# Performance work log

Measured on AMD Instinct MI355X. Metric: run time of the kernel, lower is better.

Reference implementation:

```python
import jax, jax.numpy as jnp
import numpy as np

D_MODEL = 1024
NHEAD = 16
HEAD_DIM = D_MODEL // NHEAD
D_FF = 4096
EPS = 1e-5


def _layernorm(x, g, b):
    mu = jnp.mean(x, axis=-1, keepdims=True)
    var = jnp.mean(jnp.square(x - mu), axis=-1, keepdims=True)
    return (x - mu) * jax.lax.rsqrt(var + EPS) * g + b


def setup_inputs() -> dict:
    key = jax.random.key(0)
    ks = jax.random.split(key, 8)

    def xavier(k, shape):
        fan_out, fan_in = shape
        lim = np.sqrt(6.0 / (fan_in + fan_out))
        return jax.random.uniform(k, shape, jnp.float32, -lim, lim)

    x = jax.random.normal(ks[0], (4, 2048, D_MODEL), jnp.float32)
    return {
        "x": x,
        "Wq": xavier(ks[1], (D_MODEL, D_MODEL)), "bq": jnp.zeros((D_MODEL,), jnp.float32),
        "Wk": xavier(ks[2], (D_MODEL, D_MODEL)), "bk": jnp.zeros((D_MODEL,), jnp.float32),
        "Wv": xavier(ks[3], (D_MODEL, D_MODEL)), "bv": jnp.zeros((D_MODEL,), jnp.float32),
        "Wo": xavier(ks[4], (D_MODEL, D_MODEL)), "bo": jnp.zeros((D_MODEL,), jnp.float32),
        "W1": xavier(ks[5], (D_FF, D_MODEL)), "b1": jnp.zeros((D_FF,), jnp.float32),
        "W2": xavier(ks[6], (D_MODEL, D_FF)), "b2": jnp.zeros((D_MODEL,), jnp.float32),
        "ln1_g": jnp.ones((D_MODEL,), jnp.float32), "ln1_b": jnp.zeros((D_MODEL,), jnp.float32),
        "ln2_g": jnp.ones((D_MODEL,), jnp.float32), "ln2_b": jnp.zeros((D_MODEL,), jnp.float32),
    }


def reference(x, Wq, bq, Wk, bk, Wv, bv, Wo, bo, W1, b1, W2, b2, ln1_g, ln1_b, ln2_g, ln2_b):
    B, T, D = x.shape
    H, Hd = NHEAD, HEAD_DIM

    # --- attention sublayer (pre-LN) ---
    residual = x
    xn = _layernorm(x, ln1_g, ln1_b)
    # torch Linear: y = x @ W.T + b
    q = (xn @ Wq.T + bq).reshape(B, T, H, Hd).transpose(0, 2, 1, 3)  # [B,H,T,Hd]
    k = (xn @ Wk.T + bk).reshape(B, T, H, Hd).transpose(0, 2, 1, 3)
    v = (xn @ Wv.T + bv).reshape(B, T, H, Hd).transpose(0, 2, 1, 3)

    scale = Hd ** -0.5
    scores = jnp.einsum('bhqd,bhkd->bhqk', q, k) * scale  # [B,H,T,T]
    attn = jax.nn.softmax(scores, axis=-1)
    out = jnp.einsum('bhqk,bhkd->bhqd', attn, v)           # [B,H,T,Hd]
    out = out.transpose(0, 2, 1, 3).reshape(B, T, D)
    out = out @ Wo.T + bo
    x = residual + out

    # --- FFN sublayer (pre-LN) ---
    residual = x
    xn = _layernorm(x, ln2_g, ln2_b)
    h = jax.nn.relu(xn @ W1.T + b1)
    h = h @ W2.T + b2
    return residual + h
```

## Files before the change

### kernel.cpp

```cpp
#include <hip/hip_runtime.h>
#include <hip/hip_bf16.h>

using bf16 = __hip_bfloat16;
typedef __attribute__((ext_vector_type(8))) short bf16x8;
typedef __attribute__((ext_vector_type(4))) float f32x4;

#define D_MODEL 1024
#define NHEAD 16
#define HEAD_DIM 64
#define D_FF 4096
#define SEQ 2048
#define NTOK 8192

__device__ __forceinline__ void gload16(const void* g, void* l) {
  __builtin_amdgcn_global_load_lds((const __attribute__((address_space(1))) void*)g,
                                   (__attribute__((address_space(3))) void*)l, 16, 0, 0);
}

__device__ __forceinline__ unsigned pkbf16(float lo, float hi) {
  unsigned r;
  asm("v_cvt_pk_bf16_f32 %0, %1, %2" : "=v"(r) : "v"(lo), "v"(hi));
  return r;
}

__device__ __forceinline__ float fexp2(float x) {
  float r;
  asm("v_exp_f32 %0, %1" : "=v"(r) : "v"(x));
  return r;
}

__device__ __forceinline__ float max3f(float a, float b, float c) {
  return fmaxf(fmaxf(a, b), c);
}

__global__ __launch_bounds__(256) void cvt_all(
    const float* __restrict__ W1, const float* __restrict__ W2,
    const float* __restrict__ Wq, const float* __restrict__ Wk,
    const float* __restrict__ Wv, const float* __restrict__ Wo,
    bf16* __restrict__ w1_b, bf16* __restrict__ w2_b,
    bf16* __restrict__ wqkv, bf16* __restrict__ wo_b) {
  const int bid = blockIdx.x;
  const float* src;
  bf16* dst;
  int lb;
  if (bid < 4096) { src = W1; dst = w1_b; lb = bid; }
  else if (bid < 8192) { src = W2; dst = w2_b; lb = bid - 4096; }
  else {
    const int j = (bid - 8192) >> 10;
    lb = (bid - 8192) & 1023;
    if (j == 0) { src = Wq; dst = wqkv; }
    else if (j == 1) { src = Wk; dst = wqkv + 1048576; }
    else if (j == 2) { src = Wv; dst = wqkv + 2097152; }
    else { src = Wo; dst = wo_b; }
  }
  const int i = (lb * 256 + threadIdx.x) * 4;
  const float4 v = *(const float4*)&src[i];
  dst[i + 0] = __float2bfloat16(v.x);
  dst[i + 1] = __float2bfloat16(v.y);
  dst[i + 2] = __float2bfloat16(v.z);
  dst[i + 3] = __float2bfloat16(v.w);
}

__global__ __launch_bounds__(256) void layernorm_kernel(
    const float* __restrict__ xin, const float* __restrict__ g,
    const float* __restrict__ bta, bf16* __restrict__ out) {
  const int row = blockIdx.x, t = threadIdx.x;
  const float4 v = *(const float4*)&xin[(size_t)row * D_MODEL + t * 4];
  float s = v.x + v.y + v.z + v.w;
#pragma unroll
  for (int m = 1; m < 64; m <<= 1) s += __shfl_xor(s, m);
  __shared__ float red[4], red2[4];
  const int w = t >> 6, l = t & 63;
  if (l == 0) red[w] = s;
  __syncthreads();
  const float mu = (red[0] + red[1] + red[2] + red[3]) * (1.f / 1024.f);
  const float d0 = v.x - mu, d1 = v.y - mu, d2 = v.z - mu, d3 = v.w - mu;
  float q = d0 * d0 + d1 * d1 + d2 * d2 + d3 * d3;
#pragma unroll
  for (int m = 1; m < 64; m <<= 1) q += __shfl_xor(q, m);
  if (l == 0) red2[w] = q;
  __syncthreads();
  const float var = (red2[0] + red2[1] + red2[2] + red2[3]) * (1.f / 1024.f);
  const float rs = rsqrtf(var + 1e-5f);
  const float4 gg = *(const float4*)&g[t * 4];
  const float4 bb = *(const float4*)&bta[t * 4];
  bf16* o = out + (size_t)row * D_MODEL + t * 4;
  o[0] = __float2bfloat16(d0 * rs * gg.x + bb.x);
  o[1] = __float2bfloat16(d1 * rs * gg.y + bb.y);
  o[2] = __float2bfloat16(d2 * rs * gg.z + bb.z);
  o[3] = __float2bfloat16(d3 * rs * gg.w + bb.w);
}

template <int MODE>
__global__ __launch_bounds__(512, 2) void gemmA(
    const bf16* __restrict__ A, const bf16* __restrict__ Bw,
    const float* __restrict__ bias0, const float* __restrict__ bias1,
    const float* __restrict__ bias2,
    void* __restrict__ out, int M, int N, int K) {
  constexpr int ASZ = 256 * 128;
  constexpr int TILE = ASZ + 256 * 128;
  __shared__ __align__(16) char smem[2 * TILE];

  const int t = threadIdx.x;
  const int l = t & 63, l15 = l & 15, l4 = (l >> 4) & 3;
  const int w = t >> 6, wm = w >> 2, wn = w & 3;
  const int gx = gridDim.x;
  const int nwg = gx * gridDim.y;
  const int bid0 = blockIdx.y * gx + blockIdx.x;
  const int bid = (bid0 & 7) * (nwg >> 3) + (bid0 >> 3);
  const int m0 = (bid / gx) * 256, n0 = (bid % gx) * 256;

  const int sr = t >> 3;
  const int scol = 8 * ((t & 7) ^ (sr & 7));
  const int swz = (l15 & 7) << 4;
  int coff[2];
  coff[0] = (l4 * 16) ^ swz;
  coff[1] = (64 + l4 * 16) ^ swz;

#define ST_A(j, kb, buf)                                          \
  gload16(&A[(size_t)(m0 + (j) * 64 + sr) * K + (kb) + scol],     \
          (void*)(smem + (buf) * TILE + (j) * 8192 + t * 16))
#define ST_B(j, kb, buf)                                          \
  gload16(&Bw[(size_t)(n0 + (j) * 64 + sr) * K + (kb) + scol],    \
          (void*)(smem + (buf) * TILE + ASZ + (j) * 8192 + t * 16))

  f32x4 acc[8][4] = {};
  const int NTm = K >> 6;

  ST_A(0, 0, 0); ST_A(2, 0, 0);
  ST_B(0, 0, 0); ST_B(1, 0, 0); ST_B(2, 0, 0); ST_B(3, 0, 0);
  ST_A(1, 0, 0); ST_A(3, 0, 0);
  asm volatile("s_waitcnt vmcnt(2)" ::: "memory");
  __builtin_amdgcn_s_barrier();

#define PHASE_A(p)                                                                 \
  {                                                                                \
    constexpr int kk = (p) & 1;                                                    \
    constexpr int mh = ((p) >> 1) * 4;                                             \
    bf16x8 af[4], bf[4];                                                           \
    _Pragma("unroll") for (int m = 0; m < 4; ++m)                                  \
      af[m] = *(const bf16x8*)(cb + (wm * 128 + (mh + m) * 16 + l15) * 128 +       \
                               coff[kk]);                                          \
    _Pragma("unroll") for (int n = 0; n < 4; ++n)                                  \
      bf[n] = *(const bf16x8*)(cb + ASZ + (wn * 64 + n * 16 + l15) * 128 +         \
                               coff[kk]);                                          \
    if (hasNext) {                                                                 \
      if ((p) == 0) { ST_A(0, kbn, nb); ST_A(2, kbn, nb); }                        \
      else if ((p) == 1) { ST_B(0, kbn, nb); ST_B(1, kbn, nb); }                   \
      else if ((p) == 2) { ST_B(2, kbn, nb); ST_B(3, kbn, nb); }                   \
      else { ST_A(1, kbn, nb); ST_A(3, kbn, nb); }                                 \
    }                                                                              \
    __builtin_amdgcn_s_barrier();                                                  \
    asm volatile("s_waitcnt lgkmcnt(0)" ::: "memory");                             \
    __builtin_amdgcn_sched_barrier(0);                                             \
    __builtin_amdgcn_s_setprio(1);                                                 \
    _Pragma("unroll") for (int m = 0; m < 4; ++m)                                  \
      _Pragma("unroll") for (int n = 0; n < 4; ++n)                                \
        acc[mh + m][n] = __builtin_amdgcn_mfma_f32_16x16x32_bf16(                  \
            af[m], bf[n], acc[mh + m][n], 0, 0, 0);                                \
    __builtin_amdgcn_s_setprio(0);                                                 \
    if ((p) == 1) {                                                                \
      if (hasNext) asm volatile("s_waitcnt vmcnt(4)" ::: "memory");                \
      else asm volatile("s_waitcnt vmcnt(0)" ::: "memory");                        \
    }                                                                              \
    if ((p) == 3 && hasNext)                                                       \
      asm volatile("s_waitcnt vmcnt(2)" ::: "memory");                             \
    __builtin_amdgcn_s_barrier();                                                  \
  }

  for (int kt = 0; kt < NTm; ++kt) {
    const char* cb = smem + (kt & 1) * TILE;
    const int nb = (kt & 1) ^ 1;
    const int kbn = (kt + 1) << 6;
    const bool hasNext = (kt + 1 < NTm);
    PHASE_A(0) PHASE_A(1) PHASE_A(2) PHASE_A(3)
  }
#undef PHASE_A
#undef ST_A
#undef ST_B

#pragma unroll
  for (int mf = 0; mf < 8; ++mf) {
#pragma unroll
    for (int nf = 0; nf < 4; ++nf) {
      const int col = n0 + wn * 64 + nf * 16 + l15;
      float bb;
      if constexpr (MODE == 0) {
        const int sel = col >> 10;
        const float* bp = (sel == 0) ? bias0 : ((sel == 1) ? bias1 : bias2);
        bb = bp[col & 1023];
      } else {
        bb = bias0[col];
      }
#pragma unroll
      for (int r = 0; r < 4; ++r) {
        const int row = m0 + wm * 128 + mf * 16 + l4 * 4 + r;
        float y = acc[mf][nf][r] + bb;
        if constexpr (MODE == 1) y = fmaxf(y, 0.f);
        if constexpr (MODE == 0) {
          const int sel = col >> 10;
          const int c10 = col & 1023;
          const size_t dst = (size_t)sel * (NTOK * 1024) +
                             (size_t)((row >> 11) * NHEAD + (c10 >> 6)) * (SEQ * HEAD_DIM) +
                             (size_t)(row & (SEQ - 1)) * HEAD_DIM + (c10 & 63);
          ((bf16*)out)[dst] = __float2bfloat16(y);
        } else {
          ((bf16*)out)[(size_t)row * N + col] = __float2bfloat16(y);
        }
      }
    }
  }
}

__global__ __launch_bounds__(512, 2) void gemmB(
    const bf16* __restrict__ A, const bf16* __restrict__ Bw,
    const float* __restrict__ bias, const float* __restrict__ res,
    float* __restrict__ out, int M, int N, int K) {
  constexpr int ASZ = 128 * 128;
  constexpr int TILE = ASZ + 256 * 128;
  __shared__ __align__(16) char smem[3 * TILE];

  const int t = threadIdx.x;
  const int l = t & 63, l15 = l & 15, l4 = (l >> 4) & 3;
  const int w = t >> 6, wm = w >> 2, wn = w & 3;
  const int gx = gridDim.x;
  const int nwg = gx * gridDim.y;
  const int bid0 = blockIdx.y * gx + blockIdx.x;
  const int bid = (bid0 & 7) * (nwg >> 3) + (bid0 >> 3);
  const int m0 = (bid / gx) * 128, n0 = (bid % gx) * 256;

  const int sr = t >> 3;
  const int scol = 8 * ((t & 7) ^ (sr & 7));
  const int swz = (l15 & 7) << 4;
  int coff[2];
  coff[0] = (l4 * 16) ^ swz;
  coff[1] = (64 + l4 * 16) ^ swz;

#define ST_A(j, kb, buf)                                          \
  gload16(&A[(size_t)(m0 + (j) * 64 + sr) * K + (kb) + scol],     \
          (void*)(smem + (buf) * TILE + (j) * 8192 + t * 16))
#define ST_B(j, kb, buf)                                          \
  gload16(&Bw[(size_t)(n0 + (j) * 64 + sr) * K + (kb) + scol],    \
          (void*)(smem + (buf) * TILE + ASZ + (j) * 8192 + t * 16))

  f32x4 acc[4][4] = {};
  const int NTm = K >> 6;

  ST_B(0, 0, 0); ST_B(1, 0, 0); ST_B(2, 0, 0);
  ST_B(3, 0, 0); ST_A(0, 0, 0); ST_A(1, 0, 0);
  ST_B(0, 64, 1); ST_B(1, 64, 1); ST_B(2, 64, 1);
  ST_B(3, 64, 1); ST_A(0, 64, 1); ST_A(1, 64, 1);
  asm volatile("s_waitcnt vmcnt(6)" ::: "memory");
  __builtin_amdgcn_s_barrier();

#define PHASE_B(p)                                                                 \
  {                                                                                \
    constexpr int kk = (p);                                                        \
    bf16x8 af[4], bf[4];                                                           \
    _Pragma("unroll") for (int m = 0; m < 4; ++m)                                  \
      af[m] = *(const bf16x8*)(cb + (wm * 64 + m * 16 + l15) * 128 + coff[kk]);    \
    _Pragma("unroll") for (int n = 0; n < 4; ++n)                                  \
      bf[n] = *(const bf16x8*)(cb + ASZ + (wn * 64 + n * 16 + l15) * 128 +         \
                               coff[kk]);                                          \
    if (iss) {                                                                     \
      if ((p) == 0) { ST_B(0, kbn, nb); ST_B(1, kbn, nb); ST_B(2, kbn, nb); }      \
      else { ST_B(3, kbn, nb); ST_A(0, kbn, nb); ST_A(1, kbn, nb); }               \
    }                                                                              \
    __builtin_amdgcn_s_barrier();                                                  \
    asm volatile("s_waitcnt lgkmcnt(0)" ::: "memory");                             \
    __builtin_amdgcn_sched_barrier(0);                                             \
    __builtin_amdgcn_s_setprio(1);                                                 \
    _Pragma("unroll") for (int m = 0; m < 4; ++m)                                  \
      _Pragma("unroll") for (int n = 0; n < 4; ++n)                                \
        acc[m][n] = __builtin_amdgcn_mfma_f32_16x16x32_bf16(                       \
            af[m], bf[n], acc[m][n], 0, 0, 0);                                     \
    __builtin_amdgcn_s_setprio(0);                                                 \
    if ((p) == 1) {                                                                \
      if (iss) asm volatile("s_waitcnt vmcnt(6)" ::: "memory");                    \
      else asm volatile("s_waitcnt vmcnt(0)" ::: "memory");                        \
    }                                                                              \
    __builtin_amdgcn_s_barrier();                                                  \
  }

  for (int kt = 0; kt < NTm; ++kt) {
    const char* cb = smem + (kt % 3) * TILE;
    const int nb = (kt + 2) % 3;
    const int kbn = (kt + 2) << 6;
    const bool iss = (kt + 2 < NTm);
    PHASE_B(0) PHASE_B(1)
  }
#undef PHASE_B
#undef ST_A
#undef ST_B

#pragma unroll
  for (int mf = 0; mf < 4; ++mf) {
#pragma unroll
    for (int nf = 0; nf < 4; ++nf) {
      const int col = n0 + wn * 64 + nf * 16 + l15;
      const float bb = bias[col];
#pragma unroll
      for (int r = 0; r < 4; ++r) {
        const int row = m0 + wm * 64 + mf * 16 + l4 * 4 + r;
        out[(size_t)row * N + col] = acc[mf][nf][r] + bb + res[(size_t)row * N + col];
      }
    }
  }
}

#define SCL 0.18033688011112042f
#define NT (SEQ / 64)

__global__ __launch_bounds__(512) void flash_attn(
    const bf16* __restrict__ Q, const bf16* __restrict__ K,
    const bf16* __restrict__ V, bf16* __restrict__ O) {
  __shared__ char smem[32768];
  const int t = threadIdx.x;
  const int w = t >> 6, l = t & 63;
  const int l15 = l & 15, l4 = l >> 4;
  const int bid0 = blockIdx.y * 8 + blockIdx.x;
  const int bid = (bid0 & 7) * 64 + (bid0 >> 3);
  const int bx = bid & 7, bh = bid >> 3;
  const size_t base = (size_t)bh * (SEQ * HEAD_DIM);
  const int q0 = bx * 256 + w * 32;

  int krow[4], kswz[4];
#pragma unroll
  for (int ni = 0; ni < 4; ++ni) {
    const int kr = (ni >> 1) * 32 + (ni & 1) * 4 + (l15 >> 2) * 8 + (l15 & 3);
    krow[ni] = kr * 128;
    kswz[ni] = ((kr & 3) | (((kr >> 3) & 1) << 2)) << 4;
  }

  bf16x8 qf[2][2];
#pragma unroll
  for (int mi = 0; mi < 2; ++mi)
#pragma unroll
    for (int kk = 0; kk < 2; ++kk)
      qf[mi][kk] = *(const bf16x8*)&Q[base + (size_t)(q0 + mi * 16 + l15) * 64 + kk * 32 + l4 * 8];

  bf16x8 ones;
#pragma unroll
  for (int j = 0; j < 8; ++j) ones[j] = (short)0x3F80;

  f32x4 accO[2][4] = {};
  float m_run[2], l_run[2];
#pragma unroll
  for (int mi = 0; mi < 2; ++mi) { m_run[mi] = -1e30f; l_run[mi] = 0.f; }

  short vg[8];

  const int r0 = t >> 3;
  const int c0 = 8 * ((t & 7) ^ ((r0 & 3) | (((r0 >> 3) & 1) << 2)));
  const short* kg = (const short*)K + base + r0 * 64 + c0;
  const int dv = t & 63;
  const int kb8 = (t >> 6) * 8;
  const short* vp = (const short*)V + base + (size_t)kb8 * 64 + dv;
  const int vtbyte = dv * 128 + ((kb8 * 2) ^ ((dv & 7) << 4));

#define STAGE_K(bufofs)                                          \
  {                                                              \
    gload16(kg, (void*)(smem + (bufofs) + w * 1024));            \
    kg += 4096;                                                  \
  }

#define V_GATHER()                                               \
  {                                                              \
    _Pragma("unroll") for (int j_ = 0; j_ < 8; ++j_)             \
        vg[j_] = vp[j_ * 64];                                    \
    vp += 4096;                                                  \
  }

#define VT_WRITE(bufofs)                                         \
  {                                                              \
    bf16x8 vv;                                                   \
    _Pragma("unroll") for (int j_ = 0; j_ < 8; ++j_)             \
        vv[j_] = vg[j_];                                         \
    *(bf16x8*)(smem + (bufofs) + vtbyte) = vv;                   \
  }

  STAGE_K(0);
  V_GATHER();
  VT_WRITE(16384);
  __syncthreads();

  for (int it = 0; it < NT; ++it) {
    const int cur = it & 1;
    const char* Kb = (const char*)smem + cur * 8192;
    const char* Vb = (const char*)smem + 16384 + cur * 8192;
    const bool pre = (it + 1 < NT);
    if (pre) {
      STAGE_K((cur ^ 1) * 8192);
      V_GATHER();
    }

    bf16x8 kf[2][4];
#pragma unroll
    for (int kk = 0; kk < 2; ++kk)
#pragma unroll
      for (int ni = 0; ni < 4; ++ni)
        kf[kk][ni] = *(const bf16x8*)(Kb + krow[ni] + ((kk * 64 + l4 * 16) ^ kswz[ni]));

    unsigned pw[2][8];
#pragma unroll
    for (int mi = 0; mi < 2; ++mi) {
      f32x4 s[4] = {};
      __builtin_amdgcn_s_setprio(1);
#pragma unroll
      for (int kk = 0; kk < 2; ++kk)
#pragma unroll
        for (int ni = 0; ni < 4; ++ni)
          s[ni] = __builtin_amdgcn_mfma_f32_16x16x32_bf16(kf[kk][ni], qf[mi][kk], s[ni], 0, 0, 0);
      __builtin_amdgcn_s_setprio(0);

      const float t0 = max3f(s[0][0], s[0][1], s[0][2]);
      const float t1 = max3f(s[0][3], s[1][0], s[1][1]);
      const float t2 = max3f(s[1][2], s[1][3], s[2][0]);
      const float t3 = max3f(s[2][1], s[2][2], s[2][3]);
      const float t4 = max3f(s[3][0], s[3][1], s[3][2]);
      float mx = fmaxf(max3f(t1, t2, t3), fmaxf(t4, fmaxf(t0, s[3][3])));
      mx = fmaxf(mx, __shfl_xor(mx, 16));
      mx = fmaxf(mx, __shfl_xor(mx, 32));
      const float mxs = mx * SCL;
      if (__any(mxs > m_run[mi] + 8.f)) {
        const float mn = fmaxf(m_run[mi], mxs);
        const float c = fexp2(m_run[mi] - mn);
        m_run[mi] = mn;
        l_run[mi] *= c;
#pragma unroll
        for (int ni = 0; ni < 4; ++ni)
#pragma unroll
          for (int r = 0; r < 4; ++r) accO[mi][ni][r] *= c;
      }
#pragma unroll
      for (int ni = 0; ni < 4; ++ni)
#pragma unroll
        for (int r = 0; r < 4; ++r)
          s[ni][r] = fexp2(fmaf(s[ni][r], SCL, -m_run[mi]));
#pragma unroll
      for (int kk = 0; kk < 2; ++kk)
#pragma unroll
        for (int jj = 0; jj < 4; ++jj) {
          const int ni = 2 * kk + (jj >> 1);
          pw[mi][kk * 4 + jj] = pkbf16(s[ni][2 * (jj & 1)], s[ni][2 * (jj & 1) + 1]);
        }
    }

    f32x4 zz[2] = {};
#pragma unroll
    for (int kk = 0; kk < 2; ++kk) {
      bf16x8 vf[4];
#pragma unroll
      for (int ni = 0; ni < 4; ++ni)
        vf[ni] = *(const bf16x8*)(Vb + (ni * 16 + l15) * 128 +
                                  ((kk * 64 + l4 * 16) ^ ((l15 & 7) << 4)));
#pragma unroll
      for (int mi = 0; mi < 2; ++mi) {
        union { unsigned u[4]; bf16x8 h; } pb;
#pragma unroll
        for (int jj = 0; jj < 4; ++jj) pb.u[jj] = pw[mi][kk * 4 + jj];
        __builtin_amdgcn_s_setprio(1);
#pragma unroll
        for (int ni = 0; ni < 4; ++ni)
          accO[mi][ni] = __builtin_amdgcn_mfma_f32_16x16x32_bf16(vf[ni], pb.h, accO[mi][ni], 0, 0, 0);
        zz[mi] = __builtin_amdgcn_mfma_f32_16x16x32_bf16(ones, pb.h, zz[mi], 0, 0, 0);
        __builtin_amdgcn_s_setprio(0);
      }
    }
#pragma unroll
    for (int mi = 0; mi < 2; ++mi) l_run[mi] += zz[mi][0];

    if (pre) VT_WRITE(16384 + (cur ^ 1) * 8192);
    __syncthreads();
  }

  char* ob = smem + w * 4096;
#pragma unroll
  for (int mi = 0; mi < 2; ++mi) {
    const float inv = 1.f / l_run[mi];
    const int qr = mi * 16 + l15;
    const int sw = (qr & 7) << 4;
#pragma unroll
    for (int ni = 0; ni < 4; ++ni)
#pragma unroll
      for (int rr = 0; rr < 2; ++rr) {
        const unsigned pk = pkbf16(accO[mi][ni][2 * rr] * inv, accO[mi][ni][2 * rr + 1] * inv);
        *(unsigned*)(ob + qr * 128 + ((ni * 32 + l4 * 8 + 4 * rr) ^ sw)) = pk;
      }
  }
  asm volatile("s_waitcnt lgkmcnt(0)" ::: "memory");
  __builtin_amdgcn_sched_barrier(0);

  const int b = bh >> 4, h = bh & 15;
  const int hr = l >> 1, hf = l & 1;
  const size_t orow = ((size_t)b * SEQ + bx * 256 + w * 32 + hr) * D_MODEL + h * HEAD_DIM + hf * 32;
#pragma unroll
  for (int c = 0; c < 4; ++c) {
    bf16x8 vv = *(const bf16x8*)(ob + hr * 128 + (((hf * 64) + c * 16) ^ ((hr & 7) << 4)));
    *(bf16x8*)&O[orow + c * 8] = vv;
  }
}

extern "C" void kernel_launch(void* const* d_in, const int* in_sizes, int n_in,
                              void* d_out, int out_size, void* d_ws, size_t ws_size,
                              hipStream_t stream) {
  const float* x     = (const float*)d_in[0];
  const float* Wq    = (const float*)d_in[1];
  const float* bq    = (const float*)d_in[2];
  const float* Wk    = (const float*)d_in[3];
  const float* bk    = (const float*)d_in[4];
  const float* Wv    = (const float*)d_in[5];
  const float* bv    = (const float*)d_in[6];
  const float* Wo    = (const float*)d_in[7];
  const float* bo    = (const float*)d_in[8];
  const float* W1    = (const float*)d_in[9];
  const float* b1    = (const float*)d_in[10];
  const float* W2    = (const float*)d_in[11];
  const float* b2    = (const float*)d_in[12];
  const float* ln1_g = (const float*)d_in[13];
  const float* ln1_b = (const float*)d_in[14];
  const float* ln2_g = (const float*)d_in[15];
  const float* ln2_b = (const float*)d_in[16];

  const size_t MB = 1ull << 20;
  char* ws = (char*)d_ws;
  bf16* wqkv = (bf16*)(ws + 0 * MB);
  bf16* wo_b = (bf16*)(ws + 6 * MB);
  bf16* w1_b = (bf16*)(ws + 8 * MB);
  bf16* w2_b = (bf16*)(ws + 16 * MB);
  bf16* xn   = (bf16*)(ws + 24 * MB);
  bf16* qb   = (bf16*)(ws + 40 * MB);
  bf16* kbuf = (bf16*)(ws + 56 * MB);
  bf16* vb   = (bf16*)(ws + 72 * MB);
  bf16* hb   = (bf16*)(ws + 40 * MB);
  float* x1  = (float*)(ws + 104 * MB);

  cvt_all<<<12288, 256, 0, stream>>>(W1, W2, Wq, Wk, Wv, Wo, w1_b, w2_b, wqkv, wo_b);

  layernorm_kernel<<<NTOK, 256, 0, stream>>>(x, ln1_g, ln1_b, xn);

  gemmA<0><<<dim3(3072 / 256, NTOK / 256), 512, 0, stream>>>(
      xn, wqkv, bq, bk, bv, qb, NTOK, 3072, 1024);

  flash_attn<<<dim3(SEQ / 256, 4 * NHEAD), 512, 0, stream>>>(qb, kbuf, vb, xn);

  gemmB<<<dim3(1024 / 256, NTOK / 128), 512, 0, stream>>>(
      xn, wo_b, bo, x, x1, NTOK, 1024, 1024);

  layernorm_kernel<<<NTOK, 256, 0, stream>>>(x1, ln2_g, ln2_b, xn);

  gemmA<1><<<dim3(D_FF / 256, NTOK / 256), 512, 0, stream>>>(
      xn, w1_b, b1, b1, b1, hb, NTOK, D_FF, 1024);

  gemmB<<<dim3(1024 / 256, NTOK / 128), 512, 0, stream>>>(
      hb, w2_b, b2, x1, (float*)d_out, NTOK, 1024, D_FF);
}
```

Measured before the change: 385.9 us.

## Software-pipeline attention loop to overlap QK softmax with previous PV MFMAs

Restructures the flash-attention inner loop so that each step computes QK^T and the softmax for the current K tile, then issues the PV MFMAs for the previous tile, using ping-pong probability registers. The loop is manually unrolled by two with a prologue and an epilogue. The running-sum scalar is folded into the zz accumulator, which is now rescaled together with accO. The aim is to hide exp/max latency behind matrix-core work from the other tile, at the cost of more live registers (two probability sets) and more code size.

Result: no change. 389.0 us (+0.8%).

```diff
diff --git a/kernel.cpp b/kernel.cpp
--- a/kernel.cpp
+++ b/kernel.cpp
@@ -344,10 +344,12 @@
   for (int j = 0; j < 8; ++j) ones[j] = (short)0x3F80;
 
   f32x4 accO[2][4] = {};
-  float m_run[2], l_run[2];
-#pragma unroll
-  for (int mi = 0; mi < 2; ++mi) { m_run[mi] = -1e30f; l_run[mi] = 0.f; }
-
+  f32x4 zz[2] = {};
+  float m_run[2];
+#pragma unroll
+  for (int mi = 0; mi < 2; ++mi) m_run[mi] = -1e30f;
+
+  unsigned pwA[2][8], pwB[2][8];
   short vg[8];
 
   const int r0 = t >> 3;
@@ -379,74 +381,99 @@
     *(bf16x8*)(smem + (bufofs) + vtbyte) = vv;                   \
   }
 
+#define PV_PREV(CUR, PWR)                                                         \
+  {                                                                               \
+    const char* Vb = (const char*)smem + 16384 + ((CUR) ^ 1) * 8192;              \
+    _Pragma("unroll") for (int kk = 0; kk < 2; ++kk) {                            \
+      bf16x8 vf[4];                                                               \
+      _Pragma("unroll") for (int ni = 0; ni < 4; ++ni)                            \
+        vf[ni] = *(const bf16x8*)(Vb + (ni * 16 + l15) * 128 +                    \
+                                  ((kk * 64 + l4 * 16) ^ ((l15 & 7) << 4)));      \
+      _Pragma("unroll") for (int mi = 0; mi < 2; ++mi) {                          \
+        union { unsigned u[4]; bf16x8 h; } pb;                                    \
+        _Pragma("unroll") for (int jj = 0; jj < 4; ++jj)                          \
+          pb.u[jj] = PWR[mi][kk * 4 + jj];                                        \
+        __builtin_amdgcn_s_setprio(1);                                            \
+        _Pragma("unroll") for (int ni = 0; ni < 4; ++ni)                          \
+          accO[mi][ni] = __builtin_amdgcn_mfma_f32_16x16x32_bf16(                 \
+              vf[ni], pb.h, accO[mi][ni], 0, 0, 0);                               \
+        zz[mi] = __builtin_amdgcn_mfma_f32_16x16x32_bf16(ones, pb.h,              \
+                                                         zz[mi], 0, 0, 0);        \
+        __builtin_amdgcn_s_setprio(0);                                            \
+      }                                                                           \
+    }                                                                             \
+  }
+
+#define FBODY(CUR, PWW, PWR, DO_PV, DO_STAGE, DO_VT)                              \
+  {                                                                               \
+    if (DO_VT) { VT_WRITE(16384 + (CUR) * 8192); }                                \
+    const char* Kb = (const char*)smem + (CUR) * 8192;                            \
+    bf16x8 kf[2][4];                                                              \
+    _Pragma("unroll") for (int kk = 0; kk < 2; ++kk)                              \
+      _Pragma("unroll") for (int ni = 0; ni < 4; ++ni)                            \
+        kf[kk][ni] = *(const bf16x8*)(Kb + krow[ni] +                             \
+                                      ((kk * 64 + l4 * 16) ^ kswz[ni]));          \
+    float corr[2];                                                                \
+    bool rsf[2];                                                                  \
+    _Pragma("unroll") for (int mi = 0; mi < 2; ++mi) {                            \
+      f32x4 s[4] = {};                                                            \
+      __builtin_amdgcn_s_setprio(1);                                              \
+      _Pragma("unroll") for (int kk = 0; kk < 2; ++kk)                            \
+        _Pragma("unroll") for (int ni = 0; ni < 4; ++ni)                          \
+          s[ni] = __builtin_amdgcn_mfma_f32_16x16x32_bf16(kf[kk][ni],             \
+                    qf[mi][kk], s[ni], 0, 0, 0);                                  \
+      __builtin_amdgcn_s_setprio(0);                                              \
+      const float u0 = max3f(s[0][0], s[0][1], s[0][2]);                          \
+      const float u1 = max3f(s[0][3], s[1][0], s[1][1]);                          \
+      const float u2 = max3f(s[1][2], s[1][3], s[2][0]);                          \
+      const float u3 = max3f(s[2][1], s[2][2], s[2][3]);                          \
+      const float u4 = max3f(s[3][0], s[3][1], s[3][2]);                          \
+      float mx = fmaxf(max3f(u1, u2, u3), fmaxf(u4, fmaxf(u0, s[3][3])));         \
+      mx = fmaxf(mx, __shfl_xor(mx, 16));                                         \
+      mx = fmaxf(mx, __shfl_xor(mx, 32));                                         \
+      const float mxs = mx * SCL;                                                 \
+      rsf[mi] = __any(mxs > m_run[mi] + 8.f);                                     \
+      if (rsf[mi]) {                                                              \
+        const float mn = fmaxf(m_run[mi], mxs);                                   \
+        corr[mi] = fexp2(m_run[mi] - mn);                                         \
+        m_run[mi] = mn;                                                           \
+      }                                                                           \
+      _Pragma("unroll") for (int ni = 0; ni < 4; ++ni)                            \
+        _Pragma("unroll") for (int r = 0; r < 4; ++r)                             \
+          s[ni][r] = fexp2(fmaf(s[ni][r], SCL, -m_run[mi]));                      \
+      _Pragma("unroll") for (int kk = 0; kk < 2; ++kk)                            \
+        _Pragma("unroll") for (int jj = 0; jj < 4; ++jj) {                        \
+          const int ni = 2 * kk + (jj >> 1);                                      \
+          PWW[mi][kk * 4 + jj] = pkbf16(s[ni][2 * (jj & 1)],                      \
+                                        s[ni][2 * (jj & 1) + 1]);                 \
+        }                                                                         \
+    }                                                                             \
+    if (DO_PV) { PV_PREV(CUR, PWR) }                                              \
+    if (DO_STAGE) { STAGE_K(((CUR) ^ 1) * 8192); V_GATHER(); }                    \
+    _Pragma("unroll") for (int mi = 0; mi < 2; ++mi)                              \
+      if (rsf[mi]) {                                                              \
+        _Pragma("unroll") for (int ni = 0; ni < 4; ++ni)                          \
+          _Pragma("unroll") for (int r = 0; r < 4; ++r)                           \
+            accO[mi][ni][r] *= corr[mi];                                          \
+        _Pragma("unroll") for (int r = 0; r < 4; ++r) zz[mi][r] *= corr[mi];      \
+      }                                                                           \
+    __syncthreads();                                                              \
+  }
+
   STAGE_K(0);
   V_GATHER();
   VT_WRITE(16384);
   __syncthreads();
 
-  for (int it = 0; it < NT; ++it) {
-    const int cur = it & 1;
-    const char* Kb = (const char*)smem + cur * 8192;
-    const char* Vb = (const char*)smem + 16384 + cur * 8192;
-    const bool pre = (it + 1 < NT);
-    if (pre) {
-      STAGE_K((cur ^ 1) * 8192);
-      V_GATHER();
-    }
-
-    bf16x8 kf[2][4];
-#pragma unroll
-    for (int kk = 0; kk < 2; ++kk)
-#pragma unroll
-      for (int ni = 0; ni < 4; ++ni)
-        kf[kk][ni] = *(const bf16x8*)(Kb + krow[ni] + ((kk * 64 + l4 * 16) ^ kswz[ni]));
-
-    unsigned pw[2][8];
-#pragma unroll
-    for (int mi = 0; mi < 2; ++mi) {
-      f32x4 s[4] = {};
-      __builtin_amdgcn_s_setprio(1);
-#pragma unroll
-      for (int kk = 0; kk < 2; ++kk)
-#pragma unroll
-        for (int ni = 0; ni < 4; ++ni)
-          s[ni] = __builtin_amdgcn_mfma_f32_16x16x32_bf16(kf[kk][ni], qf[mi][kk], s[ni], 0, 0, 0);
-      __builtin_amdgcn_s_setprio(0);
-
-      const float t0 = max3f(s[0][0], s[0][1], s[0][2]);
-      const float t1 = max3f(s[0][3], s[1][0], s[1][1]);
-      const float t2 = max3f(s[1][2], s[1][3], s[2][0]);
-      const float t3 = max3f(s[2][1], s[2][2], s[2][3]);
-      const float t4 = max3f(s[3][0], s[3][1], s[3][2]);
-      float mx = fmaxf(max3f(t1, t2, t3), fmaxf(t4, fmaxf(t0, s[3][3])));
-      mx = fmaxf(mx, __shfl_xor(mx, 16));
-      mx = fmaxf(mx, __shfl_xor(mx, 32));
-      const float mxs = mx * SCL;
-      if (__any(mxs > m_run[mi] + 8.f)) {
-        const float mn = fmaxf(m_run[mi], mxs);
-        const float c = fexp2(m_run[mi] - mn);
-        m_run[mi] = mn;
-        l_run[mi] *= c;
-#pragma unroll
-        for (int ni = 0; ni < 4; ++ni)
-#pragma unroll
-          for (int r = 0; r < 4; ++r) accO[mi][ni][r] *= c;
-      }
-#pragma unroll
-      for (int ni = 0; ni < 4; ++ni)
-#pragma unroll
-        for (int r = 0; r < 4; ++r)
-          s[ni][r] = fexp2(fmaf(s[ni][r], SCL, -m_run[mi]));
-#pragma unroll
-      for (int kk = 0; kk < 2; ++kk)
-#pragma unroll
-        for (int jj = 0; jj < 4; ++jj) {
-          const int ni = 2 * kk + (jj >> 1);
-          pw[mi][kk * 4 + jj] = pkbf16(s[ni][2 * (jj & 1)], s[ni][2 * (jj & 1) + 1]);
-        }
-    }
-
-    f32x4 zz[2] = {};
+  FBODY(0, pwA, pwB, false, true, false)
+  for (int it2 = 0; it2 < 15; ++it2) {
+    FBODY(1, pwB, pwA, true, true, true)
+    FBODY(0, pwA, pwB, true, true, true)
+  }
+  FBODY(1, pwB, pwA, true, false, true)
+
+  {
+    const char* Vb = (const char*)smem + 16384 + 8192;
 #pragma unroll
     for (int kk = 0; kk < 2; ++kk) {
       bf16x8 vf[4];
@@ -458,7 +485,7 @@
       for (int mi = 0; mi < 2; ++mi) {
         union { unsigned u[4]; bf16x8 h; } pb;
 #pragma unroll
-        for (int jj = 0; jj < 4; ++jj) pb.u[jj] = pw[mi][kk * 4 + jj];
+        for (int jj = 0; jj < 4; ++jj) pb.u[jj] = pwB[mi][kk * 4 + jj];
         __builtin_amdgcn_s_setprio(1);
 #pragma unroll
         for (int ni = 0; ni < 4; ++ni)
@@ -467,17 +494,13 @@
         __builtin_amdgcn_s_setprio(0);
       }
     }
-#pragma unroll
-    for (int mi = 0; mi < 2; ++mi) l_run[mi] += zz[mi][0];
-
-    if (pre) VT_WRITE(16384 + (cur ^ 1) * 8192);
-    __syncthreads();
-  }
+  }
+  __syncthreads();
 
   char* ob = smem + w * 4096;
 #pragma unroll
   for (int mi = 0; mi < 2; ++mi) {
-    const float inv = 1.f / l_run[mi];
+    const float inv = 1.f / zz[mi][0];
     const int qr = mi * 16 + l15;
     const int sw = (qr & 7) << 4;
 #pragma unroll
```
